# Kernel tuning notes

Measured on AMD Instinct MI355X. Metric: run time of the kernel, lower is better.

## Reference

```python
import jax, jax.numpy as jnp
import numpy as np

B, L, E, H = 4, 2048, 1024, 16
D = E // H


def setup_inputs() -> dict:
    key = jax.random.key(0)
    k1, k2, k3, k4 = jax.random.split(key, 4)
    x = jax.random.normal(k1, (B, L, E), dtype=jnp.float32)
    s = 1.0 / np.sqrt(E)
    w_qkv = jax.random.normal(k2, (E, 3 * E), dtype=jnp.float32) * s
    w_proj = jax.random.normal(k3, (E, E), dtype=jnp.float32) * s
    b_proj = jax.random.normal(k4, (E,), dtype=jnp.float32) * 0.01
    return {"x": x, "w_qkv": w_qkv, "w_proj": w_proj, "b_proj": b_proj}


def reference(x, w_qkv, w_proj, b_proj):
    b, l, e = x.shape
    qkv = x @ w_qkv                                  # [B,L,3E]
    q, k, v = jnp.split(qkv, 3, axis=-1)
    # 'b n (h d) -> b h n d'
    q = q.reshape(b, l, H, D).transpose(0, 2, 1, 3)
    k = k.reshape(b, l, H, D).transpose(0, 2, 1, 3)
    v = v.reshape(b, l, H, D).transpose(0, 2, 1, 3)
    scale = jnp.sqrt(jnp.asarray(e, dtype=x.dtype))  # NOTE: sqrt(E), as in source
    att = jnp.einsum('bhqd,bhkd->bhqk', q, k) / scale
    att = jax.nn.softmax(att, axis=-1)
    out = jnp.einsum('bhqk,bhkd->bhqd', att, v)
    out = out.transpose(0, 2, 1, 3).reshape(b, l, e)  # 'b h n d -> b n (h d)'
    return out @ w_proj + b_proj
```

## Files before the change

### kernel.cpp

```cpp
#include <hip/hip_runtime.h>
#include <math.h>

typedef unsigned short u16;
typedef unsigned int u32;
typedef __attribute__((ext_vector_type(4))) short s4v;
typedef __attribute__((ext_vector_type(8))) short s8v;
typedef __attribute__((ext_vector_type(4))) float f4v;

constexpr int Bn = 4;
constexpr int Ln = 2048;
constexpr int En = 1024;
constexpr int Hn = 16;
constexpr int Dn = 64;
constexpr int Mn = Bn * Ln;
constexpr int QKV_N = 3 * En;

constexpr float QSCALE_F = 0.04511175463f;

__device__ inline u16 f2bf(float f) {
    union { float f; unsigned u; } v; v.f = f;
    unsigned r = v.u + 0x7FFFu + ((v.u >> 16) & 1u);
    return (u16)(r >> 16);
}
__device__ inline u32 cvtpk(float lo, float hi) {
    u32 r;
    asm("v_cvt_pk_bf16_f32 %0, %1, %2" : "=v"(r) : "v"(lo), "v"(hi));
    return r;
}
__device__ inline s8v cat(s4v a, s4v b) {
    s8v r;
    r[0]=a[0]; r[1]=a[1]; r[2]=a[2]; r[3]=a[3];
    r[4]=b[0]; r[5]=b[1]; r[6]=b[2]; r[7]=b[3];
    return r;
}
__device__ inline s8v ldfrag(const u16* p) {
    s4v a = *(const s4v*)p;
    s4v b = *(const s4v*)(p + 16);
    return cat(a, b);
}
__device__ inline void gload_lds16(const u16* g, u16* l) {
    __builtin_amdgcn_global_load_lds(
        (const __attribute__((address_space(1))) void*)g,
        (__attribute__((address_space(3))) void*)l, 16, 0, 0);
}

__global__ __launch_bounds__(256) void cvt_bf16(
    const float* __restrict__ in, u16* __restrict__ outp, int n8)
{
    const int i = blockIdx.x * 256 + threadIdx.x;
    if (i >= n8) return;
    float4 f0 = *(const float4*)(in + (size_t)i * 8);
    float4 f1 = *(const float4*)(in + (size_t)i * 8 + 4);
    s8v v;
    v[0] = (short)f2bf(f0.x); v[1] = (short)f2bf(f0.y);
    v[2] = (short)f2bf(f0.z); v[3] = (short)f2bf(f0.w);
    v[4] = (short)f2bf(f1.x); v[5] = (short)f2bf(f1.y);
    v[6] = (short)f2bf(f1.z); v[7] = (short)f2bf(f1.w);
    *(s8v*)&outp[(size_t)i * 8] = v;
}

__global__ __launch_bounds__(256) void transT(
    const float* __restrict__ W, int K, int N, u16* __restrict__ T)
{
    __shared__ float tile[64][65];
    const int t  = threadIdx.x;
    const int kb = blockIdx.y * 64;
    const int nb = blockIdx.x * 64;
    const int r  = t >> 2;
    const int c4 = (t & 3) * 16;

    const float* wp = W + (size_t)(kb + r) * N + nb + c4;
    #pragma unroll
    for (int i = 0; i < 4; ++i) {
        float4 v = *(const float4*)(wp + 4 * i);
        tile[r][c4 + 4 * i + 0] = v.x; tile[r][c4 + 4 * i + 1] = v.y;
        tile[r][c4 + 4 * i + 2] = v.z; tile[r][c4 + 4 * i + 3] = v.w;
    }
    __syncthreads();

    s8v hv[2];
    #pragma unroll
    for (int c = 0; c < 2; ++c)
        #pragma unroll
        for (int j = 0; j < 8; ++j)
            hv[c][j] = (short)f2bf(tile[c4 + c * 8 + j][r]);
    u16* th = T + (size_t)(nb + r) * K + kb + c4;
    *(s8v*)th = hv[0]; *(s8v*)(th + 8) = hv[1];
}

template <bool OUT_BF16, bool QPRE>
__global__ __launch_bounds__(256) void gemm_bf16(
    const u16* __restrict__ A, int lda,
    const u16* __restrict__ BT, int ldb,
    float* __restrict__ C, u16* __restrict__ Cb, int ldc,
    const float* __restrict__ bias, int K)
{
    __shared__ __align__(16) u16 As[128 * 32];
    __shared__ __align__(16) u16 Bs[128 * 32];

    const int t    = threadIdx.x;
    const int lane = t & 63;
    const int w    = t >> 6;
    const int l15  = lane & 15;
    const int lg   = lane >> 4;
    const int wr   = w >> 1;
    const int wc   = w & 1;
    const int m0   = blockIdx.y * 128;
    const int n0   = blockIdx.x * 128;

    f4v acc[4][4];
    #pragma unroll
    for (int m = 0; m < 4; ++m)
        #pragma unroll
        for (int n = 0; n < 4; ++n) acc[m][n] = (f4v){0.f, 0.f, 0.f, 0.f};

    for (int k0 = 0; k0 < K; k0 += 32) {
        __syncthreads();
        #pragma unroll
        for (int i = 0; i < 2; ++i) {
            const int s   = i * 256 + t;
            const int ub  = (i * 256 + w * 64) * 8;
            const int row = s >> 2, ch = s & 3;
            gload_lds16(A  + (size_t)(m0 + row) * lda + k0 + ch * 8, As + ub);
            gload_lds16(BT + (size_t)(n0 + row) * ldb + k0 + ch * 8, Bs + ub);
        }
        __syncthreads();

        s8v fa[4], fb[4];
        #pragma unroll
        for (int m = 0; m < 4; ++m)
            fa[m] = *(const s8v*)&As[(wr * 64 + m * 16 + l15) * 32 + lg * 8];
        #pragma unroll
        for (int n = 0; n < 4; ++n)
            fb[n] = *(const s8v*)&Bs[(wc * 64 + n * 16 + l15) * 32 + lg * 8];
        #pragma unroll
        for (int m = 0; m < 4; ++m)
            #pragma unroll
            for (int n = 0; n < 4; ++n)
                acc[m][n] = __builtin_amdgcn_mfma_f32_16x16x32_bf16(fa[m], fb[n], acc[m][n], 0, 0, 0);
    }

    if (OUT_BF16) {
        #pragma unroll
        for (int m = 0; m < 4; ++m)
            #pragma unroll
            for (int n = 0; n < 4; ++n) {
                const int col = n0 + wc * 64 + n * 16 + l15;
                const float sc = (QPRE && col < En) ? QSCALE_F : 1.0f;
                #pragma unroll
                for (int r = 0; r < 4; ++r) {
                    const size_t row = m0 + wr * 64 + m * 16 + lg * 4 + r;
                    Cb[row * ldc + col] = f2bf(acc[m][n][r] * sc);
                }
            }
    } else {
        #pragma unroll
        for (int n = 0; n < 4; ++n) {
            const int col = n0 + wc * 64 + n * 16 + l15;
            const float bv = bias[col];
            #pragma unroll
            for (int m = 0; m < 4; ++m)
                #pragma unroll
                for (int r = 0; r < 4; ++r) {
                    const size_t row = m0 + wr * 64 + m * 16 + lg * 4 + r;
                    C[row * ldc + col] = acc[m][n][r] + bv;
                }
        }
    }
}

__global__ __launch_bounds__(512) void flash_bf16(u16* __restrict__ qkv)
{
    __shared__ __align__(16) u16 lds[8704];
    u16* Ks = lds;
    u16* Vt = lds + 4352;

    const int t    = threadIdx.x;
    const int lane = t & 63;
    const int w    = t >> 6;
    const int l15  = lane & 15;
    const int lg   = lane >> 4;

    const int bh = blockIdx.x;
    const int b  = bh >> 4;
    const int h  = bh & 15;
    const int q0 = blockIdx.y * 256;

    const size_t rowB = (size_t)b * Ln;

    s8v qf[2][2];
    #pragma unroll
    for (int qb = 0; qb < 2; ++qb) {
        const size_t qrow = (rowB + q0 + w * 32 + qb * 16 + l15) * QKV_N + h * Dn;
        #pragma unroll
        for (int ks = 0; ks < 2; ++ks)
            qf[qb][ks] = ldfrag(qkv + qrow + ks * 32 + lg * 4);
    }

    f4v o[2][4];
    float lpart[2] = {0.f, 0.f};
    #pragma unroll
    for (int qb = 0; qb < 2; ++qb)
        #pragma unroll
        for (int db = 0; db < 4; ++db) o[qb][db] = (f4v){0.f, 0.f, 0.f, 0.f};

    const bool isK = (w < 4);
    const int t4   = t & 255;
    const int sr   = t4 >> 2;
    const int sc   = (t4 & 3) * 16;
    const int vr   = (t4 >> 6) * 16 + (t4 & 7) * 2;
    const int vc   = ((t4 >> 3) & 7) * 8;

    for (int k0 = 0; k0 < Ln; k0 += 64) {
        s8v x0, x1;
        if (isK) {
            const size_t krow = (rowB + k0 + sr) * QKV_N + En + h * Dn + sc;
            x0 = *(const s8v*)(qkv + krow);
            x1 = *(const s8v*)(qkv + krow + 8);
        } else {
            const u16* vp = qkv + (rowB + k0 + vr) * QKV_N + 2 * En + h * Dn + vc;
            x0 = *(const s8v*)vp;
            x1 = *(const s8v*)(vp + QKV_N);
        }

        __syncthreads();
        if (isK) {
            *(s8v*)&Ks[sr * 68 + sc]     = x0;
            *(s8v*)&Ks[sr * 68 + sc + 8] = x1;
        } else {
            #pragma unroll
            for (int i = 0; i < 8; ++i) {
                u32 dw = (u32)(u16)x0[i] | ((u32)(u16)x1[i] << 16);
                *(u32*)&Vt[(vc + i) * 68 + vr] = dw;
            }
        }
        __syncthreads();

        f4v st[2][4];
        __builtin_amdgcn_s_setprio(1);
        #pragma unroll
        for (int c = 0; c < 4; ++c) {
            s8v kf0 = ldfrag(&Ks[(c * 16 + l15) * 68 + lg * 4]);
            s8v kf1 = ldfrag(&Ks[(c * 16 + l15) * 68 + 32 + lg * 4]);
            #pragma unroll
            for (int qb = 0; qb < 2; ++qb) {
                f4v acc = (f4v){0.f, 0.f, 0.f, 0.f};
                acc = __builtin_amdgcn_mfma_f32_16x16x32_bf16(kf0, qf[qb][0], acc, 0, 0, 0);
                acc = __builtin_amdgcn_mfma_f32_16x16x32_bf16(kf1, qf[qb][1], acc, 0, 0, 0);
                st[qb][c] = acc;
            }
        }
        __builtin_amdgcn_s_setprio(0);

        s8v pa[2][2];
        #pragma unroll
        for (int qb = 0; qb < 2; ++qb) {
            float p[4][4];
            #pragma unroll
            for (int c = 0; c < 4; ++c)
                #pragma unroll
                for (int r = 0; r < 4; ++r)
                    p[c][r] = __builtin_amdgcn_exp2f(st[qb][c][r]);
            float s0 = (p[0][0] + p[0][1]) + (p[0][2] + p[0][3]);
            float s1 = (p[1][0] + p[1][1]) + (p[1][2] + p[1][3]);
            float s2 = (p[2][0] + p[2][1]) + (p[2][2] + p[2][3]);
            float s3 = (p[3][0] + p[3][1]) + (p[3][2] + p[3][3]);
            lpart[qb] += (s0 + s1) + (s2 + s3);
            union { s8v s; u32 u[4]; } a0, a1;
            a0.u[0] = cvtpk(p[0][0], p[0][1]);
            a0.u[1] = cvtpk(p[0][2], p[0][3]);
            a0.u[2] = cvtpk(p[1][0], p[1][1]);
            a0.u[3] = cvtpk(p[1][2], p[1][3]);
            a1.u[0] = cvtpk(p[2][0], p[2][1]);
            a1.u[1] = cvtpk(p[2][2], p[2][3]);
            a1.u[2] = cvtpk(p[3][0], p[3][1]);
            a1.u[3] = cvtpk(p[3][2], p[3][3]);
            pa[qb][0] = a0.s;
            pa[qb][1] = a1.s;
        }

        __builtin_amdgcn_s_setprio(1);
        #pragma unroll
        for (int db = 0; db < 4; ++db) {
            s8v vf0 = ldfrag(&Vt[(db * 16 + l15) * 68 + lg * 4]);
            s8v vf1 = ldfrag(&Vt[(db * 16 + l15) * 68 + 32 + lg * 4]);
            #pragma unroll
            for (int qb = 0; qb < 2; ++qb) {
                f4v acc = o[qb][db];
                acc = __builtin_amdgcn_mfma_f32_16x16x32_bf16(pa[qb][0], vf0, acc, 0, 0, 0);
                acc = __builtin_amdgcn_mfma_f32_16x16x32_bf16(pa[qb][1], vf1, acc, 0, 0, 0);
                o[qb][db] = acc;
            }
        }
        __builtin_amdgcn_s_setprio(0);
    }

    #pragma unroll
    for (int qb = 0; qb < 2; ++qb) {
        lpart[qb] += __shfl_xor(lpart[qb], 16);
        lpart[qb] += __shfl_xor(lpart[qb], 32);
    }
    __syncthreads();
    float* sred = (float*)lds;
    if (lg == 0) {
        sred[w * 32 + l15]      = lpart[0];
        sred[w * 32 + 16 + l15] = lpart[1];
    }
    __syncthreads();

    #pragma unroll
    for (int qb = 0; qb < 2; ++qb) {
        float inv[4];
        #pragma unroll
        for (int r = 0; r < 4; ++r)
            inv[r] = 1.0f / sred[w * 32 + qb * 16 + lg * 4 + r];
        #pragma unroll
        for (int db = 0; db < 4; ++db)
            #pragma unroll
            for (int r = 0; r < 4; ++r) {
                const size_t idx =
                    (rowB + q0 + w * 32 + qb * 16 + lg * 4 + r) * QKV_N + h * Dn + db * 16 + l15;
                qkv[idx] = f2bf(o[qb][db][r] * inv[r]);
            }
    }
}

extern "C" void kernel_launch(void* const* d_in, const int* in_sizes, int n_in,
                              void* d_out, int out_size, void* d_ws, size_t ws_size,
                              hipStream_t stream)
{
    const float* x      = (const float*)d_in[0];
    const float* w_qkv  = (const float*)d_in[1];
    const float* w_proj = (const float*)d_in[2];
    const float* b_proj = (const float*)d_in[3];
    float* out = (float*)d_out;

    u16* xb  = (u16*)d_ws;
    u16* qkv = xb  + (size_t)Mn * En;
    u16* wqT = qkv + (size_t)Mn * QKV_N;
    u16* wpT = wqT + (size_t)QKV_N * En;

    cvt_bf16<<<(Mn * En / 8 + 255) / 256, 256, 0, stream>>>(x, xb, Mn * En / 8);
    transT<<<dim3(QKV_N / 64, En / 64), 256, 0, stream>>>(w_qkv, En, QKV_N, wqT);
    transT<<<dim3(En / 64, En / 64), 256, 0, stream>>>(w_proj, En, En, wpT);

    gemm_bf16<true, true><<<dim3(QKV_N / 128, Mn / 128), 256, 0, stream>>>(
        xb, En, wqT, En, nullptr, qkv, QKV_N, nullptr, En);

    flash_bf16<<<dim3(Bn * Hn, Ln / 256), 512, 0, stream>>>(qkv);

    gemm_bf16<false, false><<<dim3(En / 128, Mn / 128), 256, 0, stream>>>(
        qkv, QKV_N, wpT, En, out, nullptr, En, b_proj, En);
}
```

Before: 196.8 us.

## Double-buffer K/V tiles in LDS for flash attention loop

Doubles the shared-memory buffer so the next K/V tile is loaded from global memory during the current tile's compute and stored into the alternate buffer afterwards. This drops one of the two barriers per iteration and hides global load latency behind the MFMA work. In exchange it doubles LDS use per block, which may reduce occupancy, and holds the prefetched registers live across the compute.

Measured after the change: 209.6 us. +6.5%, slower.

```diff
diff --git a/kernel.cpp b/kernel.cpp
--- a/kernel.cpp
+++ b/kernel.cpp
@@ -171,9 +171,7 @@
 
 __global__ __launch_bounds__(512) void flash_bf16(u16* __restrict__ qkv)
 {
-    __shared__ __align__(16) u16 lds[8704];
-    u16* Ks = lds;
-    u16* Vt = lds + 4352;
+    __shared__ __align__(16) u16 lds[17408];
 
     const int t    = threadIdx.x;
     const int lane = t & 63;
@@ -192,9 +190,8 @@
     #pragma unroll
     for (int qb = 0; qb < 2; ++qb) {
         const size_t qrow = (rowB + q0 + w * 32 + qb * 16 + l15) * QKV_N + h * Dn;
-        #pragma unroll
-        for (int ks = 0; ks < 2; ++ks)
-            qf[qb][ks] = ldfrag(qkv + qrow + ks * 32 + lg * 4);
+        qf[qb][0] = ldfrag(qkv + qrow + lg * 4);
+        qf[qb][1] = ldfrag(qkv + qrow + 32 + lg * 4);
     }
 
     f4v o[2][4];
@@ -211,37 +208,54 @@
     const int vr   = (t4 >> 6) * 16 + (t4 & 7) * 2;
     const int vc   = ((t4 >> 3) & 7) * 8;
 
-    for (int k0 = 0; k0 < Ln; k0 += 64) {
+    const u16* kvbase = qkv + rowB * QKV_N + En + h * Dn;
+
+    if (isK) {
+        const u16* kp = kvbase + (size_t)sr * QKV_N + sc;
+        s8v x0 = *(const s8v*)kp;
+        s8v x1 = *(const s8v*)(kp + 8);
+        *(s8v*)&lds[sr * 68 + sc]     = x0;
+        *(s8v*)&lds[sr * 68 + sc + 8] = x1;
+    } else {
+        const u16* vp = kvbase + (size_t)vr * QKV_N + En + vc;
+        s8v x0 = *(const s8v*)vp;
+        s8v x1 = *(const s8v*)(vp + QKV_N);
+        #pragma unroll
+        for (int i = 0; i < 8; ++i) {
+            u32 dw = (u32)(u16)x0[i] | ((u32)(u16)x1[i] << 16);
+            *(u32*)&lds[4352 + (vc + i) * 68 + vr] = dw;
+        }
+    }
+    __syncthreads();
+
+    constexpr int NT = Ln / 64;
+
+    for (int kt = 0; kt < NT; ++kt) {
+        u16* Kc = lds + (kt & 1) * 8704;
+        u16* Vc = Kc + 4352;
+        u16* Kn = lds + ((kt + 1) & 1) * 8704;
+        u16* Vn = Kn + 4352;
+        const bool has_next = (kt + 1) < NT;
+
         s8v x0, x1;
-        if (isK) {
-            const size_t krow = (rowB + k0 + sr) * QKV_N + En + h * Dn + sc;
-            x0 = *(const s8v*)(qkv + krow);
-            x1 = *(const s8v*)(qkv + krow + 8);
-        } else {
-            const u16* vp = qkv + (rowB + k0 + vr) * QKV_N + 2 * En + h * Dn + vc;
-            x0 = *(const s8v*)vp;
-            x1 = *(const s8v*)(vp + QKV_N);
-        }
-
-        __syncthreads();
-        if (isK) {
-            *(s8v*)&Ks[sr * 68 + sc]     = x0;
-            *(s8v*)&Ks[sr * 68 + sc + 8] = x1;
-        } else {
-            #pragma unroll
-            for (int i = 0; i < 8; ++i) {
-                u32 dw = (u32)(u16)x0[i] | ((u32)(u16)x1[i] << 16);
-                *(u32*)&Vt[(vc + i) * 68 + vr] = dw;
-            }
-        }
-        __syncthreads();
+        if (has_next) {
+            if (isK) {
+                const u16* kp = kvbase + ((size_t)(kt + 1) * 64 + sr) * QKV_N + sc;
+                x0 = *(const s8v*)kp;
+                x1 = *(const s8v*)(kp + 8);
+            } else {
+                const u16* vp = kvbase + ((size_t)(kt + 1) * 64 + vr) * QKV_N + En + vc;
+                x0 = *(const s8v*)vp;
+                x1 = *(const s8v*)(vp + QKV_N);
+            }
+        }
 
         f4v st[2][4];
         __builtin_amdgcn_s_setprio(1);
         #pragma unroll
         for (int c = 0; c < 4; ++c) {
-            s8v kf0 = ldfrag(&Ks[(c * 16 + l15) * 68 + lg * 4]);
-            s8v kf1 = ldfrag(&Ks[(c * 16 + l15) * 68 + 32 + lg * 4]);
+            s8v kf0 = ldfrag(&Kc[(c * 16 + l15) * 68 + lg * 4]);
+            s8v kf1 = ldfrag(&Kc[(c * 16 + l15) * 68 + 32 + lg * 4]);
             #pragma unroll
             for (int qb = 0; qb < 2; ++qb) {
                 f4v acc = (f4v){0.f, 0.f, 0.f, 0.f};
@@ -282,8 +296,8 @@
         __builtin_amdgcn_s_setprio(1);
         #pragma unroll
         for (int db = 0; db < 4; ++db) {
-            s8v vf0 = ldfrag(&Vt[(db * 16 + l15) * 68 + lg * 4]);
-            s8v vf1 = ldfrag(&Vt[(db * 16 + l15) * 68 + 32 + lg * 4]);
+            s8v vf0 = ldfrag(&Vc[(db * 16 + l15) * 68 + lg * 4]);
+            s8v vf1 = ldfrag(&Vc[(db * 16 + l15) * 68 + 32 + lg * 4]);
             #pragma unroll
             for (int qb = 0; qb < 2; ++qb) {
                 f4v acc = o[qb][db];
@@ -293,6 +307,20 @@
             }
         }
         __builtin_amdgcn_s_setprio(0);
+
+        if (has_next) {
+            if (isK) {
+                *(s8v*)&Kn[sr * 68 + sc]     = x0;
+                *(s8v*)&Kn[sr * 68 + sc + 8] = x1;
+            } else {
+                #pragma unroll
+                for (int i = 0; i < 8; ++i) {
+                    u32 dw = (u32)(u16)x0[i] | ((u32)(u16)x1[i] << 16);
+                    *(u32*)&Vn[(vc + i) * 68 + vr] = dw;
+                }
+            }
+        }
+        __syncthreads();
     }
 
     #pragma unroll
@@ -300,7 +328,6 @@
         lpart[qb] += __shfl_xor(lpart[qb], 16);
         lpart[qb] += __shfl_xor(lpart[qb], 32);
     }
-    __syncthreads();
     float* sred = (float*)lds;
     if (lg == 0) {
         sred[w * 32 + l15]      = lpart[0];
```

## Split flash attention over key range and combine partials in separate kernel

Applied to the files above, without the earlier changes.

Adds a split-K dimension to the attention grid so each block processes half the keys, doubling block count to improve CU occupancy. Unnormalized fp32 partial outputs and row sums are written to workspace and a new combine kernel sums them, normalizes and writes bf16 into the qkv buffer. This trades extra global memory traffic and a kernel launch for more parallelism; correctness relies on the softmax not using a per-split running max.

After: 530.4 us. +169.5%, slower.

```diff
diff --git a/kernel.cpp b/kernel.cpp
--- a/kernel.cpp
+++ b/kernel.cpp
@@ -169,7 +169,9 @@
     }
 }
 
-__global__ __launch_bounds__(512) void flash_bf16(u16* __restrict__ qkv)
+__global__ __launch_bounds__(512, 8) void flash_bf16(
+    const u16* __restrict__ qkv,
+    float* __restrict__ P0, float* __restrict__ P1, float* __restrict__ lout)
 {
     __shared__ __align__(16) u16 lds[8704];
     u16* Ks = lds;
@@ -181,20 +183,21 @@
     const int l15  = lane & 15;
     const int lg   = lane >> 4;
 
-    const int bh = blockIdx.x;
-    const int b  = bh >> 4;
-    const int h  = bh & 15;
-    const int q0 = blockIdx.y * 256;
+    const int bh    = blockIdx.x;
+    const int b     = bh >> 4;
+    const int h     = bh & 15;
+    const int q0    = blockIdx.y * 256;
+    const int split = blockIdx.z;
 
     const size_t rowB = (size_t)b * Ln;
+    float* __restrict__ Pout = split ? P1 : P0;
 
     s8v qf[2][2];
     #pragma unroll
     for (int qb = 0; qb < 2; ++qb) {
         const size_t qrow = (rowB + q0 + w * 32 + qb * 16 + l15) * QKV_N + h * Dn;
-        #pragma unroll
-        for (int ks = 0; ks < 2; ++ks)
-            qf[qb][ks] = ldfrag(qkv + qrow + ks * 32 + lg * 4);
+        qf[qb][0] = ldfrag(qkv + qrow + lg * 4);
+        qf[qb][1] = ldfrag(qkv + qrow + 32 + lg * 4);
     }
 
     f4v o[2][4];
@@ -211,7 +214,10 @@
     const int vr   = (t4 >> 6) * 16 + (t4 & 7) * 2;
     const int vc   = ((t4 >> 3) & 7) * 8;
 
-    for (int k0 = 0; k0 < Ln; k0 += 64) {
+    const int kbeg = split * (Ln / 2);
+    const int kend = kbeg + (Ln / 2);
+
+    for (int k0 = kbeg; k0 < kend; k0 += 64) {
         s8v x0, x1;
         if (isK) {
             const size_t krow = (rowB + k0 + sr) * QKV_N + En + h * Dn + sc;
@@ -300,29 +306,50 @@
         lpart[qb] += __shfl_xor(lpart[qb], 16);
         lpart[qb] += __shfl_xor(lpart[qb], 32);
     }
-    __syncthreads();
-    float* sred = (float*)lds;
     if (lg == 0) {
-        sred[w * 32 + l15]      = lpart[0];
-        sred[w * 32 + 16 + l15] = lpart[1];
-    }
-    __syncthreads();
-
-    #pragma unroll
-    for (int qb = 0; qb < 2; ++qb) {
-        float inv[4];
-        #pragma unroll
-        for (int r = 0; r < 4; ++r)
-            inv[r] = 1.0f / sred[w * 32 + qb * 16 + lg * 4 + r];
+        const size_t lrow = (size_t)split * Mn + rowB + q0 + w * 32;
+        lout[(lrow + l15) * Hn + h]      = lpart[0];
+        lout[(lrow + 16 + l15) * Hn + h] = lpart[1];
+    }
+    #pragma unroll
+    for (int qb = 0; qb < 2; ++qb)
         #pragma unroll
         for (int db = 0; db < 4; ++db)
             #pragma unroll
             for (int r = 0; r < 4; ++r) {
                 const size_t idx =
-                    (rowB + q0 + w * 32 + qb * 16 + lg * 4 + r) * QKV_N + h * Dn + db * 16 + l15;
-                qkv[idx] = f2bf(o[qb][db][r] * inv[r]);
-            }
-    }
+                    (rowB + q0 + w * 32 + qb * 16 + lg * 4 + r) * En + h * Dn + db * 16 + l15;
+                Pout[idx] = o[qb][db][r];
+            }
+}
+
+__global__ __launch_bounds__(256) void combine(
+    const float* __restrict__ P0, const float* __restrict__ P1,
+    const float* __restrict__ lbuf, u16* __restrict__ qkv, int n8)
+{
+    const int i = blockIdx.x * 256 + threadIdx.x;
+    if (i >= n8) return;
+    const size_t f = (size_t)i * 8;
+    const int q   = (int)(f >> 10);
+    const int rem = (int)(f & 1023);
+    const int h   = rem >> 6;
+    const float l0 = lbuf[(size_t)q * Hn + h];
+    const float l1 = lbuf[(size_t)Mn * Hn + (size_t)q * Hn + h];
+    const float inv = 1.0f / (l0 + l1);
+    float4 a0 = *(const float4*)(P0 + f);
+    float4 a1 = *(const float4*)(P0 + f + 4);
+    float4 b0 = *(const float4*)(P1 + f);
+    float4 b1 = *(const float4*)(P1 + f + 4);
+    s8v v;
+    v[0] = (short)f2bf((a0.x + b0.x) * inv);
+    v[1] = (short)f2bf((a0.y + b0.y) * inv);
+    v[2] = (short)f2bf((a0.z + b0.z) * inv);
+    v[3] = (short)f2bf((a0.w + b0.w) * inv);
+    v[4] = (short)f2bf((a1.x + b1.x) * inv);
+    v[5] = (short)f2bf((a1.y + b1.y) * inv);
+    v[6] = (short)f2bf((a1.z + b1.z) * inv);
+    v[7] = (short)f2bf((a1.w + b1.w) * inv);
+    *(s8v*)&qkv[(size_t)q * QKV_N + rem] = v;
 }
 
 extern "C" void kernel_launch(void* const* d_in, const int* in_sizes, int n_in,
@@ -335,10 +362,13 @@
     const float* b_proj = (const float*)d_in[3];
     float* out = (float*)d_out;
 
-    u16* xb  = (u16*)d_ws;
-    u16* qkv = xb  + (size_t)Mn * En;
-    u16* wqT = qkv + (size_t)Mn * QKV_N;
-    u16* wpT = wqT + (size_t)QKV_N * En;
+    u16*   qkv  = (u16*)d_ws;
+    u16*   wqT  = qkv + (size_t)Mn * QKV_N;
+    u16*   wpT  = wqT + (size_t)QKV_N * En;
+    float* P1   = (float*)(wpT + (size_t)En * En);
+    float* lbuf = P1 + (size_t)Mn * En;
+    float* P0   = lbuf + (size_t)2 * Mn * Hn;
+    u16*   xb   = (u16*)P0;
 
     cvt_bf16<<<(Mn * En / 8 + 255) / 256, 256, 0, stream>>>(x, xb, Mn * En / 8);
     transT<<<dim3(QKV_N / 64, En / 64), 256, 0, stream>>>(w_qkv, En, QKV_N, wqT);
@@ -347,7 +377,10 @@
     gemm_bf16<true, true><<<dim3(QKV_N / 128, Mn / 128), 256, 0, stream>>>(
         xb, En, wqT, En, nullptr, qkv, QKV_N, nullptr, En);
 
-    flash_bf16<<<dim3(Bn * Hn, Ln / 256), 512, 0, stream>>>(qkv);
+    flash_bf16<<<dim3(Bn * Hn, Ln / 256, 2), 512, 0, stream>>>(qkv, P0, P1, lbuf);
+
+    combine<<<(Mn * En / 8 + 255) / 256, 256, 0, stream>>>(
+        P0, P1, lbuf, qkv, Mn * En / 8);
 
     gemm_bf16<false, false><<<dim3(En / 128, Mn / 128), 256, 0, stream>>>(
         qkv, QKV_N, wpT, En, out, nullptr, En, b_proj, En);
```
